# Kernel tuning notes

Measured on AMD Instinct MI355X. Metric: run time of the kernel, lower is better.

## Reference

```python
import jax, jax.numpy as jnp
import numpy as np

NUM_EMBEDDINGS = 1024
EMBEDDING_DIM = 64


def setup_inputs() -> dict:
    key = jax.random.key(0)
    kx, kw = jax.random.split(key)
    x = jax.random.normal(kx, (8, 128, 128, EMBEDDING_DIM), dtype=jnp.float32)
    W = jax.random.normal(kw, (NUM_EMBEDDINGS, EMBEDDING_DIM), dtype=jnp.float32)
    return {"x": x, "W": W}


def reference(x, W):
    # Flatten to [N, D]
    flat = x.reshape(-1, EMBEDDING_DIM)
    # ||f||^2 + ||w||^2 - 2 f.w  -> [N, K]
    f_sq = jnp.sum(flat * flat, axis=1, keepdims=True)          # [N, 1]
    w_sq = jnp.sum(W * W, axis=1)                               # [K]
    prod = 2.0 * jnp.einsum('nd,kd->nk', flat, W)               # [N, K]
    distances = f_sq + w_sq - prod
    indices = jnp.argmin(distances, axis=1)                     # [N]
    # one_hot @ W is an exact gather of codebook rows
    quantized = W[indices].reshape(x.shape)
    quantized_with_grad = x + jax.lax.stop_gradient(quantized - x)
    return (quantized_with_grad, quantized, indices)
```

## Files before the change

kernel.cpp:

```cpp
#include <hip/hip_runtime.h>

#define VQ_D 64
#define VQ_MARGIN 0.015f

typedef __attribute__((ext_vector_type(8))) short bf16x8;
typedef __attribute__((ext_vector_type(4))) float f32x4;

static __device__ __forceinline__ unsigned short bf16_rne(float v) {
    unsigned u = __float_as_uint(v);
    u += 0x7fffu + ((u >> 16) & 1u);
    return (unsigned short)(u >> 16);
}

__global__ __launch_bounds__(256) void vq_prep_kernel(
    const float* __restrict__ W, unsigned short* __restrict__ Wpk,
    float* __restrict__ wsqpk, float* __restrict__ wsq,
    unsigned int* __restrict__ ctr, int K)
{
    const int t = blockIdx.x * 256 + threadIdx.x;
    if (t == 0) *ctr = 0u;
    const int NT = K >> 4;
    if (t >= NT * 64) return;
    const int ct = t >> 6;
    const int l  = t & 63;
    const int c  = ct * 16 + (l & 15);
    const int g  = l >> 4;

    const float* wr = W + (size_t)c * VQ_D;

    float s0 = 0.f, s1 = 0.f, s2 = 0.f, s3 = 0.f;
    const float4* w4 = reinterpret_cast<const float4*>(wr);
    #pragma unroll
    for (int j = 0; j < VQ_D / 4; ++j) {
        float4 v = w4[j];
        s0 = __fmaf_rn(v.x, v.x, s0); s1 = __fmaf_rn(v.y, v.y, s1);
        s2 = __fmaf_rn(v.z, v.z, s2); s3 = __fmaf_rn(v.w, v.w, s3);
    }
    const float wq = (s0 + s1) + (s2 + s3);
    wsqpk[ct * 64 + l] = wq;
    if (l < 16) wsq[ct * 16 + l] = wq;

    float v0[8], v1[8];
    {
        const float4* p0 = reinterpret_cast<const float4*>(wr + g * 8);
        const float4* p1 = reinterpret_cast<const float4*>(wr + 32 + g * 8);
        float4 a = p0[0], b = p0[1], cc = p1[0], d = p1[1];
        v0[0]=a.x; v0[1]=a.y; v0[2]=a.z; v0[3]=a.w; v0[4]=b.x; v0[5]=b.y; v0[6]=b.z; v0[7]=b.w;
        v1[0]=cc.x;v1[1]=cc.y;v1[2]=cc.z;v1[3]=cc.w;v1[4]=d.x; v1[5]=d.y; v1[6]=d.z; v1[7]=d.w;
    }
    bf16x8 h0, h1, l0, l1;
    #pragma unroll
    for (int j = 0; j < 8; ++j) {
        unsigned short hb0 = bf16_rne(v0[j]);
        unsigned short hb1 = bf16_rne(v1[j]);
        h0[j] = (short)hb0;
        h1[j] = (short)hb1;
        l0[j] = (short)bf16_rne(v0[j] - __uint_as_float((unsigned)hb0 << 16));
        l1[j] = (short)bf16_rne(v1[j] - __uint_as_float((unsigned)hb1 << 16));
    }
    bf16x8* P = reinterpret_cast<bf16x8*>(Wpk);
    P[(ct * 4 + 0) * 64 + l] = h0;
    P[(ct * 4 + 1) * 64 + l] = h1;
    P[(ct * 4 + 2) * 64 + l] = l0;
    P[(ct * 4 + 3) * 64 + l] = l1;
}

__global__ __launch_bounds__(256) void vq_mfma_kernel(
    const float* __restrict__ x, const float* __restrict__ W,
    const unsigned short* __restrict__ Wpk, const float* __restrict__ wsqpk,
    float* __restrict__ out, int* __restrict__ flags,
    unsigned int* __restrict__ ctr, int N, int K)
{
    __shared__ float sD1[4][64], sD2[4][64];
    __shared__ int   sI1[4][64];
    __shared__ int   sIdx[64];

    const int tid  = threadIdx.x;
    const int wv   = tid >> 6;
    const int lane = tid & 63;
    const int g    = lane >> 4;
    const int c16  = lane & 15;
    const int rbase = blockIdx.x * 64;

    bf16x8 xh[4][2], xl[4][2];
    #pragma unroll
    for (int s = 0; s < 4; ++s) {
        int row = rbase + s * 16 + c16;
        if (row >= N) row = N - 1;
        const float* xr = x + (size_t)row * VQ_D;
        #pragma unroll
        for (int h = 0; h < 2; ++h) {
            const float4* p = reinterpret_cast<const float4*>(xr + h * 32 + g * 8);
            float4 v0 = p[0], v1 = p[1];
            float vv[8] = {v0.x, v0.y, v0.z, v0.w, v1.x, v1.y, v1.z, v1.w};
            #pragma unroll
            for (int j = 0; j < 8; ++j) {
                unsigned short hb = bf16_rne(vv[j]);
                float hf = __uint_as_float((unsigned)hb << 16);
                xh[s][h][j] = (short)hb;
                xl[s][h][j] = (short)bf16_rne(vv[j] - hf);
            }
        }
    }

    float d1[4][4], d2[4][4]; int i1[4][4];
    #pragma unroll
    for (int s = 0; s < 4; ++s)
        #pragma unroll
        for (int i = 0; i < 4; ++i) { d1[s][i] = 3.4e38f; d2[s][i] = 3.4e38f; i1[s][i] = 0; }

    const int NT = K >> 4;
    const int t0 = wv * (NT >> 2);
    const int t1 = t0 + (NT >> 2);
    const bf16x8* __restrict__ P = reinterpret_cast<const bf16x8*>(Wpk);

    #pragma unroll 2
    for (int ct = t0; ct < t1; ++ct) {
        const int c = ct * 16 + c16;
        const int pb = ct * 256 + lane;
        bf16x8 bh0 = P[pb];
        bf16x8 bh1 = P[pb + 64];
        bf16x8 bl0 = P[pb + 128];
        bf16x8 bl1 = P[pb + 192];
        const float wq = wsqpk[ct * 64 + lane];

        #pragma unroll
        for (int s = 0; s < 4; ++s) {
            f32x4 acc = {0.f, 0.f, 0.f, 0.f};
            acc = __builtin_amdgcn_mfma_f32_16x16x32_bf16(xh[s][0], bh0, acc, 0, 0, 0);
            acc = __builtin_amdgcn_mfma_f32_16x16x32_bf16(xh[s][1], bh1, acc, 0, 0, 0);
            acc = __builtin_amdgcn_mfma_f32_16x16x32_bf16(xl[s][0], bh0, acc, 0, 0, 0);
            acc = __builtin_amdgcn_mfma_f32_16x16x32_bf16(xl[s][1], bh1, acc, 0, 0, 0);
            acc = __builtin_amdgcn_mfma_f32_16x16x32_bf16(xh[s][0], bl0, acc, 0, 0, 0);
            acc = __builtin_amdgcn_mfma_f32_16x16x32_bf16(xh[s][1], bl1, acc, 0, 0, 0);
            #pragma unroll
            for (int i = 0; i < 4; ++i) {
                float d = __fmaf_rn(-2.0f, acc[i], wq);
                float o1 = d1[s][i];
                d2[s][i] = fminf(d2[s][i], fmaxf(d, o1));
                bool lt = d < o1;
                d1[s][i] = lt ? d : o1;
                i1[s][i] = lt ? c : i1[s][i];
            }
        }
    }

    #pragma unroll
    for (int s = 0; s < 4; ++s)
        #pragma unroll
        for (int i = 0; i < 4; ++i) {
            float a1 = d1[s][i], a2 = d2[s][i]; int ai = i1[s][i];
            #pragma unroll
            for (int m = 1; m < 16; m <<= 1) {
                float o1 = __shfl_xor(a1, m, 64);
                float o2 = __shfl_xor(a2, m, 64);
                int   oi = __shfl_xor(ai, m, 64);
                float n1 = fminf(a1, o1);
                a2 = fminf(fminf(a2, o2), fmaxf(a1, o1));
                ai = (o1 < a1) ? oi : ai;
                a1 = n1;
            }
            if (c16 == 0) {
                int r = s * 16 + g * 4 + i;
                sD1[wv][r] = a1; sD2[wv][r] = a2; sI1[wv][r] = ai;
            }
        }
    __syncthreads();

    if (tid < 64) {
        int row = rbase + tid;
        float m1 = sD1[0][tid], m2 = sD2[0][tid]; int mi = sI1[0][tid];
        #pragma unroll
        for (int w = 1; w < 4; ++w) {
            float a = sD1[w][tid], b = sD2[w][tid]; int ii = sI1[w][tid];
            if (a < m1) { m2 = fminf(m1, b); mi = ii; m1 = a; }
            else        { m2 = fminf(m2, a); }
        }
        sIdx[tid] = mi;
        if (row < N) {
            out[(size_t)2 * N * VQ_D + row] = (float)mi;
            if (m2 - m1 <= VQ_MARGIN) {
                unsigned int pos = atomicAdd(ctr, 1u);
                if (pos < (unsigned)N) flags[pos] = row;
            }
        }
    }
    __syncthreads();

    const float4* W4 = reinterpret_cast<const float4*>(W);
    const float4* X4 = reinterpret_cast<const float4*>(x);
    float4* O0 = reinterpret_cast<float4*>(out);
    float4* O1 = O0 + (size_t)N * (VQ_D / 4);
    const size_t base4 = (size_t)rbase * (VQ_D / 4);
    #pragma unroll
    for (int i = 0; i < 4; ++i) {
        int j = i * 256 + tid;
        int rowo = j >> 4;
        int d4 = j & 15;
        if (rbase + rowo < N) {
            int idx = sIdx[rowo];
            float4 w = W4[(size_t)idx * (VQ_D / 4) + d4];
            float4 xv = X4[base4 + j];
            float4 o;
            o.x = xv.x + (w.x - xv.x);
            o.y = xv.y + (w.y - xv.y);
            o.z = xv.z + (w.z - xv.z);
            o.w = xv.w + (w.w - xv.w);
            O0[base4 + j] = o;
            O1[base4 + j] = w;
        }
    }
}

__global__ __launch_bounds__(256) void vq_recheck_kernel(
    const float* __restrict__ x, const float* __restrict__ W,
    const float* __restrict__ wsq, const int* __restrict__ flags,
    const unsigned int* __restrict__ ctr, float* __restrict__ out, int N, int K)
{
    __shared__ float sBD[4];
    __shared__ int   sBI[4];
    __shared__ int   sFin;

    const int tid  = threadIdx.x;
    const int wv   = tid >> 6;
    const int lane = tid & 63;
    unsigned int cnt = *ctr;
    if (cnt > (unsigned)N) cnt = (unsigned)N;

    const float4* W4 = reinterpret_cast<const float4*>(W);
    for (unsigned int t = blockIdx.x; t < cnt; t += gridDim.x) {
        const int row = flags[t];
        float f[VQ_D];
        {
            const float4* xf = reinterpret_cast<const float4*>(x) + (size_t)row * (VQ_D / 4);
            #pragma unroll
            for (int i = 0; i < VQ_D / 4; ++i) {
                float4 v = xf[i];
                f[4 * i + 0] = v.x; f[4 * i + 1] = v.y;
                f[4 * i + 2] = v.z; f[4 * i + 3] = v.w;
            }
        }
        float s0 = 0.f, s1 = 0.f, s2 = 0.f, s3 = 0.f;
        #pragma unroll
        for (int q = 0; q < VQ_D; q += 4) {
            s0 = __fmaf_rn(f[q], f[q], s0);         s1 = __fmaf_rn(f[q + 1], f[q + 1], s1);
            s2 = __fmaf_rn(f[q + 2], f[q + 2], s2); s3 = __fmaf_rn(f[q + 3], f[q + 3], s3);
        }
        const float fsq = (s0 + s1) + (s2 + s3);

        float best = 3.4e38f; int bidx = 0x7fffffff;
        #pragma unroll
        for (int tt = 0; tt < 4; ++tt) {
            const int c = wv * (K >> 2) + tt * 64 + lane;
            const float4* wc = W4 + (size_t)c * (VQ_D / 4);
            float d0 = 0.f, dd1 = 0.f, dd2 = 0.f, dd3 = 0.f;
            #pragma unroll
            for (int i = 0; i < VQ_D / 4; ++i) {
                float4 w = wc[i];
                d0  = __fmaf_rn(f[4 * i + 0], w.x, d0);
                dd1 = __fmaf_rn(f[4 * i + 1], w.y, dd1);
                dd2 = __fmaf_rn(f[4 * i + 2], w.z, dd2);
                dd3 = __fmaf_rn(f[4 * i + 3], w.w, dd3);
            }
            float dot  = (d0 + dd1) + (dd2 + dd3);
            float dist = __fmaf_rn(-2.0f, dot, fsq + wsq[c]);
            if (dist < best || (dist == best && c < bidx)) { best = dist; bidx = c; }
        }
        #pragma unroll
        for (int m = 1; m < 64; m <<= 1) {
            float od = __shfl_xor(best, m, 64);
            int   oi = __shfl_xor(bidx, m, 64);
            if (od < best || (od == best && oi < bidx)) { best = od; bidx = oi; }
        }
        if (lane == 0) { sBD[wv] = best; sBI[wv] = bidx; }
        __syncthreads();
        if (tid == 0) {
            float m1 = sBD[0]; int mi = sBI[0];
            #pragma unroll
            for (int w = 1; w < 4; ++w) {
                float a = sBD[w]; int ii = sBI[w];
                if (a < m1 || (a == m1 && ii < mi)) { m1 = a; mi = ii; }
            }
            sFin = mi;
        }
        __syncthreads();
        const int mi = sFin;
        if (tid < 64) {
            float wvv = W[(size_t)mi * VQ_D + tid];
            float xv  = x[(size_t)row * VQ_D + tid];
            out[(size_t)row * VQ_D + tid] = xv + (wvv - xv);
            out[(size_t)N * VQ_D + (size_t)row * VQ_D + tid] = wvv;
            if (tid == 0) out[(size_t)2 * N * VQ_D + row] = (float)mi;
        }
        __syncthreads();
    }
}

__global__ __launch_bounds__(256) void vq_wsq_kernel(const float* __restrict__ W,
                                                     float* __restrict__ wsq, int K)
{
    int c = blockIdx.x * 256 + threadIdx.x;
    if (c >= K) return;
    const float4* w4 = reinterpret_cast<const float4*>(W) + (size_t)c * (VQ_D / 4);
    float s0 = 0.f, s1 = 0.f, s2 = 0.f, s3 = 0.f;
    #pragma unroll
    for (int j = 0; j < VQ_D / 4; ++j) {
        float4 v = w4[j];
        s0 = __fmaf_rn(v.x, v.x, s0); s1 = __fmaf_rn(v.y, v.y, s1);
        s2 = __fmaf_rn(v.z, v.z, s2); s3 = __fmaf_rn(v.w, v.w, s3);
    }
    wsq[c] = (s0 + s1) + (s2 + s3);
}

__global__ __launch_bounds__(256, 6) void vq_main_kernel(const float* __restrict__ x,
    const float* __restrict__ W, const float* __restrict__ wsq,
    float* __restrict__ out, int N, int K)
{
    __shared__ unsigned long long sMerge[256];
    __shared__ int sIdx[64];
    const int tid  = threadIdx.x;
    const int lane = tid & 63;
    const int rbase = blockIdx.x * 64;
    const int row  = rbase + lane;
    const int lrow = (row < N) ? row : (N - 1);
    float f[VQ_D];
    {
        const float4* xf = reinterpret_cast<const float4*>(x) + (size_t)lrow * (VQ_D / 4);
        #pragma unroll
        for (int i = 0; i < VQ_D / 4; ++i) {
            float4 v = xf[i];
            f[4 * i + 0] = v.x; f[4 * i + 1] = v.y;
            f[4 * i + 2] = v.z; f[4 * i + 3] = v.w;
        }
    }
    float fsq;
    {
        float s0 = 0.f, s1 = 0.f, s2 = 0.f, s3 = 0.f;
        #pragma unroll
        for (int q = 0; q < VQ_D; q += 4) {
            s0 = __fmaf_rn(f[q], f[q], s0);         s1 = __fmaf_rn(f[q + 1], f[q + 1], s1);
            s2 = __fmaf_rn(f[q + 2], f[q + 2], s2); s3 = __fmaf_rn(f[q + 3], f[q + 3], s3);
        }
        fsq = (s0 + s1) + (s2 + s3);
    }
    const int slice = __builtin_amdgcn_readfirstlane(tid >> 6);
    const int c0 = slice * (K >> 2);
    const int c1 = c0 + (K >> 2);
    float best = 3.4e38f;
    int bidx = c0;
    const float4* __restrict__ W4 = reinterpret_cast<const float4*>(W);
    #pragma unroll 2
    for (int c = c0; c < c1; ++c) {
        const float4* wc = W4 + (size_t)c * (VQ_D / 4);
        float d0 = 0.f, d1 = 0.f, d2 = 0.f, d3 = 0.f;
        #pragma unroll
        for (int i = 0; i < VQ_D / 4; ++i) {
            float4 w = wc[i];
            d0 = __fmaf_rn(f[4 * i + 0], w.x, d0); d1 = __fmaf_rn(f[4 * i + 1], w.y, d1);
            d2 = __fmaf_rn(f[4 * i + 2], w.z, d2); d3 = __fmaf_rn(f[4 * i + 3], w.w, d3);
        }
        float dot = (d0 + d1) + (d2 + d3);
        float dist = __fmaf_rn(-2.0f, dot, fsq + wsq[c]);
        if (dist < best) { best = dist; bidx = c; }
    }
    best = fmaxf(best, 0.0f);
    sMerge[tid] = ((unsigned long long)__float_as_uint(best) << 32) | (unsigned int)bidx;
    __syncthreads();
    if (tid < 64) {
        unsigned long long mm = sMerge[tid];
        unsigned long long a = sMerge[tid + 64];  if (a < mm) mm = a;
        unsigned long long b = sMerge[tid + 128]; if (b < mm) mm = b;
        unsigned long long d = sMerge[tid + 192]; if (d < mm) mm = d;
        int idx = (int)(mm & 0xFFFFFFFFu);
        sIdx[tid] = idx;
        if (rbase + tid < N) out[(size_t)2 * N * VQ_D + rbase + tid] = (float)idx;
    }
    __syncthreads();
    const float4* X4 = reinterpret_cast<const float4*>(x);
    float4* O0 = reinterpret_cast<float4*>(out);
    float4* O1 = O0 + (size_t)N * (VQ_D / 4);
    const size_t base4 = (size_t)rbase * (VQ_D / 4);
    #pragma unroll
    for (int i = 0; i < 4; ++i) {
        int j = i * 256 + tid;
        int rowo = j >> 4, d4 = j & 15;
        if (rbase + rowo < N) {
            int idx = sIdx[rowo];
            float4 w = W4[(size_t)idx * (VQ_D / 4) + d4];
            float4 xv = X4[base4 + j];
            float4 o;
            o.x = xv.x + (w.x - xv.x); o.y = xv.y + (w.y - xv.y);
            o.z = xv.z + (w.z - xv.z); o.w = xv.w + (w.w - xv.w);
            O0[base4 + j] = o; O1[base4 + j] = w;
        }
    }
}

extern "C" void kernel_launch(void* const* d_in, const int* in_sizes, int n_in,
                              void* d_out, int out_size, void* d_ws, size_t ws_size,
                              hipStream_t stream)
{
    const float* x = (const float*)d_in[0];
    const float* W = (const float*)d_in[1];
    float* out = (float*)d_out;
    const int N = in_sizes[0] / VQ_D;
    const int K = in_sizes[1] / VQ_D;
    const int NT = K >> 4;

    char* ws = (char*)d_ws;
    float*          wsq   = (float*)ws;
    unsigned int*   ctr   = (unsigned int*)(ws + 4096);
    int*            flags = (int*)(ws + 8192);
    unsigned short* Wpk   = (unsigned short*)(ws + 8192 + (size_t)N * 4);
    float*          wsqpk = (float*)((char*)Wpk + (size_t)K * VQ_D * 4);
    const size_t need = 8192 + (size_t)N * 4 + (size_t)K * VQ_D * 4
                      + (size_t)NT * 64 * 4;

    if (ws_size >= need && (N % 64) == 0 && (K % 256) == 0) {
        vq_prep_kernel<<<(NT * 64 + 255) / 256, 256, 0, stream>>>(W, Wpk, wsqpk,
                                                                  wsq, ctr, K);
        vq_mfma_kernel<<<N / 64, 256, 0, stream>>>(x, W, Wpk, wsqpk,
                                                   out, flags, ctr, N, K);
        vq_recheck_kernel<<<2048, 256, 0, stream>>>(x, W, wsq, flags, ctr, out, N, K);
    } else {
        vq_wsq_kernel<<<(K + 255) / 256, 256, 0, stream>>>(W, wsq, K);
        vq_main_kernel<<<(N + 63) / 64, 256, 0, stream>>>(x, W, wsq, out, N, K);
    }
}
```

Measured before the change: 178.4 us.

## Fold -2 scale and wsq into MFMA, pack tile index into distance bits

Result: slower. 296.6 us (+66.3%).

```diff
diff --git a/kernel.cpp b/kernel.cpp
--- a/kernel.cpp
+++ b/kernel.cpp
@@ -1,7 +1,7 @@
 #include <hip/hip_runtime.h>
 
 #define VQ_D 64
-#define VQ_MARGIN 0.015f
+#define VQ_MARGIN 0.025f
 
 typedef __attribute__((ext_vector_type(8))) short bf16x8;
 typedef __attribute__((ext_vector_type(4))) float f32x4;
@@ -51,12 +51,14 @@
     bf16x8 h0, h1, l0, l1;
     #pragma unroll
     for (int j = 0; j < 8; ++j) {
-        unsigned short hb0 = bf16_rne(v0[j]);
-        unsigned short hb1 = bf16_rne(v1[j]);
+        float a0 = -2.0f * v0[j];
+        float a1 = -2.0f * v1[j];
+        unsigned short hb0 = bf16_rne(a0);
+        unsigned short hb1 = bf16_rne(a1);
         h0[j] = (short)hb0;
         h1[j] = (short)hb1;
-        l0[j] = (short)bf16_rne(v0[j] - __uint_as_float((unsigned)hb0 << 16));
-        l1[j] = (short)bf16_rne(v1[j] - __uint_as_float((unsigned)hb1 << 16));
+        l0[j] = (short)bf16_rne(a0 - __uint_as_float((unsigned)hb0 << 16));
+        l1[j] = (short)bf16_rne(a1 - __uint_as_float((unsigned)hb1 << 16));
     }
     bf16x8* P = reinterpret_cast<bf16x8*>(Wpk);
     P[(ct * 4 + 0) * 64 + l] = h0;
@@ -103,11 +105,11 @@
         }
     }
 
-    float d1[4][4], d2[4][4]; int i1[4][4];
+    float d1[4][4], d2[4][4];
     #pragma unroll
     for (int s = 0; s < 4; ++s)
         #pragma unroll
-        for (int i = 0; i < 4; ++i) { d1[s][i] = 3.4e38f; d2[s][i] = 3.4e38f; i1[s][i] = 0; }
+        for (int i = 0; i < 4; ++i) { d1[s][i] = 3.4e38f; d2[s][i] = 3.4e38f; }
 
     const int NT = K >> 4;
     const int t0 = wv * (NT >> 2);
@@ -116,31 +118,30 @@
 
     #pragma unroll 2
     for (int ct = t0; ct < t1; ++ct) {
-        const int c = ct * 16 + c16;
         const int pb = ct * 256 + lane;
-        bf16x8 bh0 = P[pb];
-        bf16x8 bh1 = P[pb + 64];
-        bf16x8 bl0 = P[pb + 128];
-        bf16x8 bl1 = P[pb + 192];
+        bf16x8 vh0 = P[pb];
+        bf16x8 vh1 = P[pb + 64];
+        bf16x8 vl0 = P[pb + 128];
+        bf16x8 vl1 = P[pb + 192];
         const float wq = wsqpk[ct * 64 + lane];
+        const f32x4 cin = {wq, wq, wq, wq};
 
         #pragma unroll
         for (int s = 0; s < 4; ++s) {
-            f32x4 acc = {0.f, 0.f, 0.f, 0.f};
-            acc = __builtin_amdgcn_mfma_f32_16x16x32_bf16(xh[s][0], bh0, acc, 0, 0, 0);
-            acc = __builtin_amdgcn_mfma_f32_16x16x32_bf16(xh[s][1], bh1, acc, 0, 0, 0);
-            acc = __builtin_amdgcn_mfma_f32_16x16x32_bf16(xl[s][0], bh0, acc, 0, 0, 0);
-            acc = __builtin_amdgcn_mfma_f32_16x16x32_bf16(xl[s][1], bh1, acc, 0, 0, 0);
-            acc = __builtin_amdgcn_mfma_f32_16x16x32_bf16(xh[s][0], bl0, acc, 0, 0, 0);
-            acc = __builtin_amdgcn_mfma_f32_16x16x32_bf16(xh[s][1], bl1, acc, 0, 0, 0);
+            f32x4 acc = cin;
+            acc = __builtin_amdgcn_mfma_f32_16x16x32_bf16(xh[s][0], vh0, acc, 0, 0, 0);
+            acc = __builtin_amdgcn_mfma_f32_16x16x32_bf16(xh[s][1], vh1, acc, 0, 0, 0);
+            acc = __builtin_amdgcn_mfma_f32_16x16x32_bf16(xl[s][0], vh0, acc, 0, 0, 0);
+            acc = __builtin_amdgcn_mfma_f32_16x16x32_bf16(xl[s][1], vh1, acc, 0, 0, 0);
+            acc = __builtin_amdgcn_mfma_f32_16x16x32_bf16(xh[s][0], vl0, acc, 0, 0, 0);
+            acc = __builtin_amdgcn_mfma_f32_16x16x32_bf16(xh[s][1], vl1, acc, 0, 0, 0);
             #pragma unroll
             for (int i = 0; i < 4; ++i) {
-                float d = __fmaf_rn(-2.0f, acc[i], wq);
+                float p = __uint_as_float(
+                    (__float_as_uint(acc[i]) & 0xFFFFFFC0u) | (unsigned)ct);
                 float o1 = d1[s][i];
-                d2[s][i] = fminf(d2[s][i], fmaxf(d, o1));
-                bool lt = d < o1;
-                d1[s][i] = lt ? d : o1;
-                i1[s][i] = lt ? c : i1[s][i];
+                d2[s][i] = fminf(fmaxf(p, o1), d2[s][i]);
+                d1[s][i] = fminf(p, o1);
             }
         }
     }
@@ -149,7 +150,8 @@
     for (int s = 0; s < 4; ++s)
         #pragma unroll
         for (int i = 0; i < 4; ++i) {
-            float a1 = d1[s][i], a2 = d2[s][i]; int ai = i1[s][i];
+            float a1 = d1[s][i], a2 = d2[s][i];
+            int ai = (int)(__float_as_uint(a1) & 63u) * 16 + c16;
             #pragma unroll
             for (int m = 1; m < 16; m <<= 1) {
                 float o1 = __shfl_xor(a1, m, 64);
@@ -217,22 +219,37 @@
     const float* __restrict__ wsq, const int* __restrict__ flags,
     const unsigned int* __restrict__ ctr, float* __restrict__ out, int N, int K)
 {
-    __shared__ float sBD[4];
-    __shared__ int   sBI[4];
-    __shared__ int   sFin;
+    __shared__ float sBD[4][16];
+    __shared__ int   sBI[4][16];
+    __shared__ int   sRow[16];
+    __shared__ int   sFin[16];
 
     const int tid  = threadIdx.x;
     const int wv   = tid >> 6;
     const int lane = tid & 63;
+    const int r    = lane >> 2;
+    const int cs   = lane & 3;
     unsigned int cnt = *ctr;
     if (cnt > (unsigned)N) cnt = (unsigned)N;
 
     const float4* W4 = reinterpret_cast<const float4*>(W);
-    for (unsigned int t = blockIdx.x; t < cnt; t += gridDim.x) {
-        const int row = flags[t];
+    const float4* X4 = reinterpret_cast<const float4*>(x);
+    float4* O0 = reinterpret_cast<float4*>(out);
+    float4* O1 = O0 + (size_t)N * (VQ_D / 4);
+
+    for (unsigned int base = blockIdx.x * 16u; base < cnt; base += gridDim.x * 16u) {
+        if (tid < 16) {
+            unsigned int t = base + (unsigned)tid;
+            sRow[tid] = (t < cnt) ? flags[t] : -1;
+        }
+        __syncthreads();
+
+        const int growM = sRow[r];
+        const int row = (growM >= 0) ? growM : 0;
+
         float f[VQ_D];
         {
-            const float4* xf = reinterpret_cast<const float4*>(x) + (size_t)row * (VQ_D / 4);
+            const float4* xf = X4 + (size_t)row * (VQ_D / 4);
             #pragma unroll
             for (int i = 0; i < VQ_D / 4; ++i) {
                 float4 v = xf[i];
@@ -249,9 +266,10 @@
         const float fsq = (s0 + s1) + (s2 + s3);
 
         float best = 3.4e38f; int bidx = 0x7fffffff;
-        #pragma unroll
-        for (int tt = 0; tt < 4; ++tt) {
-            const int c = wv * (K >> 2) + tt * 64 + lane;
+        const int cb = wv * (K >> 2) + cs * 64;
+        #pragma unroll 2
+        for (int t2 = 0; t2 < 64; ++t2) {
+            const int c = cb + t2;
             const float4* wc = W4 + (size_t)c * (VQ_D / 4);
             float d0 = 0.f, dd1 = 0.f, dd2 = 0.f, dd3 = 0.f;
             #pragma unroll
@@ -264,33 +282,42 @@
             }
             float dot  = (d0 + dd1) + (dd2 + dd3);
             float dist = __fmaf_rn(-2.0f, dot, fsq + wsq[c]);
-            if (dist < best || (dist == best && c < bidx)) { best = dist; bidx = c; }
-        }
-        #pragma unroll
-        for (int m = 1; m < 64; m <<= 1) {
+            if (dist < best) { best = dist; bidx = c; }
+        }
+        #pragma unroll
+        for (int m = 1; m < 4; m <<= 1) {
             float od = __shfl_xor(best, m, 64);
             int   oi = __shfl_xor(bidx, m, 64);
             if (od < best || (od == best && oi < bidx)) { best = od; bidx = oi; }
         }
-        if (lane == 0) { sBD[wv] = best; sBI[wv] = bidx; }
+        if (cs == 0) { sBD[wv][r] = best; sBI[wv][r] = bidx; }
         __syncthreads();
-        if (tid == 0) {
-            float m1 = sBD[0]; int mi = sBI[0];
+
+        if (tid < 16 && sRow[tid] >= 0) {
+            float m1 = sBD[0][tid]; int mi = sBI[0][tid];
             #pragma unroll
             for (int w = 1; w < 4; ++w) {
-                float a = sBD[w]; int ii = sBI[w];
+                float a = sBD[w][tid]; int ii = sBI[w][tid];
                 if (a < m1 || (a == m1 && ii < mi)) { m1 = a; mi = ii; }
             }
-            sFin = mi;
+            sFin[tid] = mi;
+            out[(size_t)2 * N * VQ_D + sRow[tid]] = (float)mi;
         }
         __syncthreads();
-        const int mi = sFin;
-        if (tid < 64) {
-            float wvv = W[(size_t)mi * VQ_D + tid];
-            float xv  = x[(size_t)row * VQ_D + tid];
-            out[(size_t)row * VQ_D + tid] = xv + (wvv - xv);
-            out[(size_t)N * VQ_D + (size_t)row * VQ_D + tid] = wvv;
-            if (tid == 0) out[(size_t)2 * N * VQ_D + row] = (float)mi;
+
+        {
+            int rowo = tid >> 4, d4 = tid & 15;
+            int grow = sRow[rowo];
+            if (grow >= 0) {
+                int idx = sFin[rowo];
+                float4 w  = W4[(size_t)idx * (VQ_D / 4) + d4];
+                float4 xv = X4[(size_t)grow * (VQ_D / 4) + d4];
+                float4 o;
+                o.x = xv.x + (w.x - xv.x); o.y = xv.y + (w.y - xv.y);
+                o.z = xv.z + (w.z - xv.z); o.w = xv.w + (w.w - xv.w);
+                O0[(size_t)grow * (VQ_D / 4) + d4] = o;
+                O1[(size_t)grow * (VQ_D / 4) + d4] = w;
+            }
         }
         __syncthreads();
     }
@@ -416,12 +443,12 @@
     const size_t need = 8192 + (size_t)N * 4 + (size_t)K * VQ_D * 4
                       + (size_t)NT * 64 * 4;
 
-    if (ws_size >= need && (N % 64) == 0 && (K % 256) == 0) {
+    if (ws_size >= need && (N % 64) == 0 && (K % 256) == 0 && NT <= 64) {
         vq_prep_kernel<<<(NT * 64 + 255) / 256, 256, 0, stream>>>(W, Wpk, wsqpk,
                                                                   wsq, ctr, K);
         vq_mfma_kernel<<<N / 64, 256, 0, stream>>>(x, W, Wpk, wsqpk,
                                                    out, flags, ctr, N, K);
-        vq_recheck_kernel<<<2048, 256, 0, stream>>>(x, W, wsq, flags, ctr, out, N, K);
+        vq_recheck_kernel<<<1024, 256, 0, stream>>>(x, W, wsq, flags, ctr, out, N, K);
     } else {
         vq_wsq_kernel<<<(K + 255) / 256, 256, 0, stream>>>(W, wsq, K);
         vq_main_kernel<<<(N + 63) / 64, 256, 0, stream>>>(x, W, wsq, out, N, K);
```
